# Kernel tuning notes

Measured on AMD Instinct MI355X. Metric: run time of the kernel, lower is better.

Reference implementation:

```python
import jax, jax.numpy as jnp
import numpy as np

PI = 3.141592653
PC_RANGE = np.array([-140.8, -40.0, -3.0, 140.8, 40.0, 1.0], np.float32)
IOU_THR = 0.1


def limit_period(val, offset=0.5, period=2 * PI):
    return val - jnp.floor(val / period + offset) * period


def pairwise_iou3d(boxes):
    # Axis-aligned 3D IoU approximation of the external boxes_iou3d_gpu CUDA kernel
    # (kernel source not provided). boxes: [N,7] = x,y,z,h,w,l,yaw; extents x<-l, y<-w, z<-h.
    c = boxes[:, :3]
    d = boxes[:, jnp.array([5, 4, 3])]
    lo = c - d * 0.5
    hi = c + d * 0.5
    inter = jnp.clip(jnp.minimum(hi[:, None, :], hi[None, :, :]) - jnp.maximum(lo[:, None, :], lo[None, :, :]), 0.0)
    inter_v = inter.prod(-1)                       # [N,N]
    vol = d.prod(-1)                               # [N]
    return inter_v / jnp.maximum(vol[:, None] + vol[None, :] - inter_v, 1e-8)


def cluster_assign(iou):
    # Greedy sequential clustering: repeatedly take the first unassigned box and
    # assign every box with iou > 0.1 (including already-assigned ones -> overwrite)
    # to a new cluster id. Equivalent to the original while-loop since an index,
    # once nonzero, never returns to zero, so the "first zero" scans left-to-right.
    iou = jax.lax.stop_gradient(iou)
    n = iou.shape[0]

    def body(i, carry):
        idx, cid = carry
        is_new = idx[i] == 0
        idx = jnp.where(is_new & (iou[i] > IOU_THR), cid, idx)
        return idx, cid + jnp.where(is_new, 1, 0).astype(jnp.int32)

    idx0 = jnp.zeros(n, jnp.int32)
    idx, cid = jax.lax.fori_loop(0, n, body, (idx0, jnp.int32(1)))
    return idx, cid


def cluster_fusion(boxes, scores, indices):
    n = boxes.shape[0]
    ids = jnp.arange(1, n + 1, dtype=jnp.int32)
    M = indices[None, :] == ids[:, None]            # [K,N] membership, K==N (padded)
    s_m = jnp.where(M, scores[None, :], 0.0)        # masked scores
    s_sum = s_m.sum(1)
    s_norm = s_m / jnp.maximum(s_sum, 1e-12)[:, None]
    dirs = boxes[:, 6]
    ref_idx = jnp.argmax(jnp.where(M, scores[None, :], -jnp.inf), axis=1)
    ref_dir = dirs[ref_idx]                         # yaw of max-score box per cluster
    diff = jnp.abs(dirs[None, :] - ref_dir[:, None])
    diff = jnp.where(diff > PI, 2 * PI - diff, diff)
    gt = diff > PI / 2
    score_gt = (s_m * gt).sum(1)
    score_le = s_sum - score_gt
    flip = jnp.where((score_gt <= score_le)[:, None], gt, ~gt)
    dirs_adj = limit_period(dirs[None, :] + PI * flip)
    theta = jnp.arctan2((jnp.sin(dirs_adj) * s_norm).sum(1), (jnp.cos(dirs_adj) * s_norm).sum(1))
    center_dim = s_norm @ boxes[:, :6]              # [K,6] score-weighted fusion
    boxes_fused = jnp.concatenate([center_dim, theta[:, None]], axis=1)
    # score fusion: sum_i s_sorted[i] ** (i+1), clipped to 1 (zeros from padding contribute 0)
    s_sorted = jnp.sort(s_m, axis=1)[:, ::-1]
    powers = jnp.arange(1, n + 1, dtype=jnp.float32)
    s_fused = jnp.minimum((s_sorted ** powers[None, :]).sum(1), 1.0)
    member = M.any(1)
    return boxes_fused, s_fused, member


def boxes_to_corners_3d(boxes):
    # order 'hwl': dims = h,w,l; l along x, w along y, h along z; rotate about z by yaw
    x, y, z = boxes[:, 0], boxes[:, 1], boxes[:, 2]
    h, w, l = boxes[:, 3], boxes[:, 4], boxes[:, 5]
    yaw = boxes[:, 6]
    xs = jnp.array([1, 1, -1, -1, 1, 1, -1, -1], jnp.float32) * 0.5
    ys = jnp.array([-1, 1, 1, -1, -1, 1, 1, -1], jnp.float32) * 0.5
    zs = jnp.array([-1, -1, -1, -1, 1, 1, 1, 1], jnp.float32) * 0.5
    cx = l[:, None] * xs
    cy = w[:, None] * ys
    cz = h[:, None] * zs
    c_, s_ = jnp.cos(yaw)[:, None], jnp.sin(yaw)[:, None]
    rx = cx * c_ - cy * s_
    ry = cx * s_ + cy * c_
    return jnp.stack([rx + x[:, None], ry + y[:, None], cz + z[:, None]], axis=-1)  # [N,8,3]


def setup_inputs() -> dict:
    key = jax.random.key(0)
    k1, k2, k3, k4, k5, k6 = jax.random.split(key, 6)
    C, M = 512, 8                # 512 objects seen by 8 agents -> 4096 detections
    N = C * M
    cx = jax.random.uniform(k1, (C,), minval=-120.0, maxval=120.0)
    cy = jax.random.uniform(k2, (C,), minval=-35.0, maxval=35.0)
    centers = jnp.stack([cx, cy, jnp.zeros(C)], -1)                     # [C,3]
    pos = (centers[:, None, :] + jax.random.normal(k3, (C, M, 3)) * 0.3).reshape(N, 3)
    dims = jnp.array([[1.56, 1.84, 4.2]]) + jax.random.normal(k4, (N, 3)) * 0.05  # h,w,l
    base_yaw = jax.random.uniform(k5, (C, 1), minval=-PI, maxval=PI)
    yaw = (base_yaw + jax.random.normal(k6, (C, M)) * 0.1).reshape(N, 1)
    boxes = jnp.concatenate([pos, dims, yaw], axis=1).astype(jnp.float32)
    scores = jax.random.uniform(jax.random.fold_in(key, 9), (N,), minval=0.05, maxval=0.95).astype(jnp.float32)
    return {"boxes": boxes, "scores": scores}


def reference(boxes, scores):
    boxes = boxes.at[:, 6].set(limit_period(boxes[:, 6]))
    iou = pairwise_iou3d(boxes)
    indices, _ = cluster_assign(iou)
    boxes_f, scores_f, member = cluster_fusion(boxes, scores, indices)
    corners = boxes_to_corners_3d(boxes_f)
    in_range = ((corners[..., 0] > PC_RANGE[0]) & (corners[..., 0] < PC_RANGE[3]) &
                (corners[..., 1] > PC_RANGE[1]) & (corners[..., 1] < PC_RANGE[4])).all(1)
    valid = member & in_range
    newid = jnp.cumsum(valid.astype(jnp.int32))     # remap surviving cluster ids to 1..K'
    safe = jnp.maximum(indices - 1, 0)
    new_indices = jnp.where((indices > 0) & valid[safe], newid[safe], 0)
    boxes_out = jnp.where(valid[:, None], boxes_f, 0.0)
    scores_out = jnp.where(valid, scores_f, 0.0)
    return boxes_out, scores_out, valid, new_indices
```

## Files before the change

kernel.cpp:

```cpp
#include <hip/hip_runtime.h>
#include <math.h>

#define PI_F      3.141592653f
#define TWO_PI_F  6.283185306f
#define HALF_PI_F 1.5707963265f
#define IOU_THR_F 0.1f

typedef unsigned long long u64;

__device__ __forceinline__ float limit_period_f(float v) {
    return v - floorf(v / TWO_PI_F + 0.5f) * TWO_PI_F;
}

__global__ void adj_kernel(const float* __restrict__ boxes,
                           u64* __restrict__ adjC,
                           unsigned char* __restrict__ occByte,
                           int* __restrict__ indices,
                           int n, int words) {
    __shared__ float jS[7][64];
    int w = blockIdx.x;
    int tid = threadIdx.x;
    int lane = tid & 63, wv = tid >> 6;
    if (blockIdx.x == 0) {
        int i2 = blockIdx.y * 256 + tid;
        if (i2 < n) indices[i2] = 0;
    }
    if (tid < 64) {
        int j = (w << 6) + tid;
        if (j < n) {
            float b0 = boxes[j*7+0], b1 = boxes[j*7+1], b2 = boxes[j*7+2];
            float b3 = boxes[j*7+3], b4 = boxes[j*7+4], b5 = boxes[j*7+5];
            jS[0][tid] = b0 - b5*0.5f;  jS[3][tid] = b0 + b5*0.5f;
            jS[1][tid] = b1 - b4*0.5f;  jS[4][tid] = b1 + b4*0.5f;
            jS[2][tid] = b2 - b3*0.5f;  jS[5][tid] = b2 + b3*0.5f;
            jS[6][tid] = (b5*b4)*b3;
        }
    }
    __syncthreads();
    int i = blockIdx.y * 256 + tid;
    u64 word = 0ull;
    if (i < n) {
        float b0 = boxes[i*7+0], b1 = boxes[i*7+1], b2 = boxes[i*7+2];
        float b3 = boxes[i*7+3], b4 = boxes[i*7+4], b5 = boxes[i*7+5];
        float lix = b0 - b5*0.5f, hix = b0 + b5*0.5f;
        float liy = b1 - b4*0.5f, hiy = b1 + b4*0.5f;
        float liz = b2 - b3*0.5f, hiz = b2 + b3*0.5f;
        float vi  = (b5*b4)*b3;
        int jmax = n - (w << 6); if (jmax > 64) jmax = 64;
        for (int jj = 0; jj < jmax; ++jj) {
            float ix = fminf(hix, jS[3][jj]) - fmaxf(lix, jS[0][jj]); ix = fmaxf(ix, 0.0f);
            float iy = fminf(hiy, jS[4][jj]) - fmaxf(liy, jS[1][jj]); iy = fmaxf(iy, 0.0f);
            float iz = fminf(hiz, jS[5][jj]) - fmaxf(liz, jS[2][jj]); iz = fmaxf(iz, 0.0f);
            float inter = (ix*iy)*iz;
            float u = fmaxf(vi + jS[6][jj] - inter, 1e-8f);
            bool pred = (inter / u) > IOU_THR_F;
            word |= ((u64)(pred ? 1 : 0)) << jj;
        }
        adjC[(size_t)w * n + i] = word;
    }
    u64 bal = __ballot((i < n) && word != 0ull);
    int rb = blockIdx.y * 4 + wv;
    if (lane == 0 && rb < 64)
        occByte[rb * 64 + w] = bal ? (unsigned char)1 : (unsigned char)0;
}

__global__ __launch_bounds__(1024) void mis_round_kernel(
        const u64* __restrict__ adjC,
        const unsigned char* __restrict__ occByte,
        u64* __restrict__ SG, u64* __restrict__ occLG,
        int* __restrict__ seedList, int* __restrict__ nclust,
        int n, int words) {
    __shared__ u64 S_l[64], R_l[64], occL[64];
    __shared__ int unresolved;
    __shared__ int wsS[64];
    int tid = threadIdx.x;
    int lane = tid & 63, wv = tid >> 6;

    for (int rb = wv; rb < 64; rb += 16) {
        unsigned char b = occByte[rb * 64 + lane];
        u64 m = __ballot(b != 0);
        if (lane == 0) occL[rb] = m;
    }
    if (tid < 64) {
        int base = tid << 6;
        int vb = n - base;
        u64 valid = (vb >= 64) ? ~0ull : ((vb <= 0) ? 0ull : ((1ull << vb) - 1ull));
        S_l[tid] = 0ull;
        R_l[tid] = ~valid;
    }
    __syncthreads();
    if (tid < 64) occLG[tid] = occL[tid];

    int id0[4], id1[4], id2[4], id3[4];
    u64 r0[4], r1[4], r2[4], r3[4], rstR[4];
    #pragma unroll
    for (int k = 0; k < 4; ++k) {
        int rb = (k << 4) + wv;
        int i = (rb << 6) + lane;
        id0[k] = id1[k] = id2[k] = id3[k] = 0xFF;
        r0[k] = r1[k] = r2[k] = r3[k] = 0ull; rstR[k] = 0ull;
        u64 lowm = lane ? ((1ull << lane) - 1ull) : 0ull;
        u64 oc = occL[rb] & ((rb >= 63) ? ~0ull : ((2ull << rb) - 1ull));
        int cnt = 0;
        while (oc) {
            int e = (int)__ffsll(oc) - 1; oc &= oc - 1;
            if (e >= words) break;
            u64 row = (i < n) ? adjC[(size_t)e * n + i] : 0ull;
            u64 em = (e < rb) ? ~0ull : lowm;
            u64 re = row & em;
            if (re) {
                if      (cnt == 0) { id0[k] = e; r0[k] = re; }
                else if (cnt == 1) { id1[k] = e; r1[k] = re; }
                else if (cnt == 2) { id2[k] = e; r2[k] = re; }
                else if (cnt == 3) { id3[k] = e; r3[k] = re; }
                else rstR[k] |= 1ull << e;
                ++cnt;
            }
        }
    }

    unsigned done = 0;
    #pragma unroll
    for (int k = 0; k < 4; ++k)
        if ((((k << 4) + wv) << 6) + lane >= n) done |= 1u << k;

    for (;;) {
        if (tid == 0) unresolved = 0;
        unsigned pendSeed = 0, pendRes = 0;
        #pragma unroll
        for (int k = 0; k < 4; ++k) {
            if (done & (1u << k)) continue;
            int rb = (k << 4) + wv;
            int i = (rb << 6) + lane;
            u64 lowm = lane ? ((1ull << lane) - 1ull) : 0ull;
            u64 sA = 0ull, uA = 0ull;
            if (id0[k] != 0xFF) { sA |= r0[k] & S_l[id0[k]]; uA |= r0[k] & ~R_l[id0[k]]; }
            if (id1[k] != 0xFF) { sA |= r1[k] & S_l[id1[k]]; uA |= r1[k] & ~R_l[id1[k]]; }
            if (id2[k] != 0xFF) { sA |= r2[k] & S_l[id2[k]]; uA |= r2[k] & ~R_l[id2[k]]; }
            if (id3[k] != 0xFF) { sA |= r3[k] & S_l[id3[k]]; uA |= r3[k] & ~R_l[id3[k]]; }
            u64 rm = rstR[k];
            while (rm) {
                int e = (int)__ffsll(rm) - 1; rm &= rm - 1;
                u64 row = adjC[(size_t)e * n + i];
                u64 em = (e < rb) ? ~0ull : lowm;
                sA |= row & S_l[e] & em;
                uA |= row & ~R_l[e] & em;
            }
            if (sA) pendRes |= 1u << k;
            else if (!uA) { pendSeed |= 1u << k; pendRes |= 1u << k; }
        }
        __syncthreads();
        #pragma unroll
        for (int k = 0; k < 4; ++k) {
            u64 bS = __ballot((pendSeed >> k) & 1u);
            u64 bR = __ballot((pendRes  >> k) & 1u);
            int rb = (k << 4) + wv;
            if (lane == 0 && rb < 64) {
                if (bS) atomicOr(&S_l[rb], bS);
                if (bR) atomicOr(&R_l[rb], bR);
            }
        }
        done |= pendRes;
        if ((done & 0xFu) != 0xFu) unresolved = 1;
        __syncthreads();
        if (unresolved == 0) break;
    }

    if (tid < 64) {
        u64 s = S_l[tid];
        SG[tid] = s;
        int pc = (int)__popcll(s);
        int x = pc;
        for (int o = 1; o < 64; o <<= 1) {
            int y = __shfl_up(x, o);
            if (tid >= o) x += y;
        }
        wsS[tid] = x - pc;
        if (tid == 63) *nclust = x;
    }
    __syncthreads();
    if (tid < 64) {
        u64 sbits = S_l[tid];
        int r = wsS[tid];
        while (sbits) {
            int b = (int)__ffsll(sbits) - 1; sbits &= sbits - 1;
            seedList[r++] = (tid << 6) + b;
        }
    }
}

__global__ void fusion_kernel(const float* __restrict__ boxes,
                              const float* __restrict__ scores,
                              const u64* __restrict__ SG,
                              const u64* __restrict__ occLG,
                              const int* __restrict__ seedListG,
                              const int* __restrict__ nclust,
                              const u64* __restrict__ adjC,
                              int* __restrict__ indices,
                              float* __restrict__ fused,
                              float* __restrict__ sfused,
                              int* __restrict__ validArr, int n, int words) {
    int lane = threadIdx.x;
    __shared__ u64 S_s[64];
    __shared__ int ws_s[64];
    __shared__ u64 occ_s[64];
    __shared__ unsigned short js[320], js2[320];
    __shared__ unsigned char keepB[320];
    __shared__ float ms[256];
    __shared__ float ds[256];
    __shared__ float bx[6][256];
    __shared__ float sv[256], cv[256], pw[256];
    __shared__ float refdirS, denomS;
    __shared__ int   flipS;
    {
        u64 s = (lane < words) ? SG[lane] : 0ull;
        S_s[lane] = s;
        occ_s[lane] = occLG[lane];
        int pc = (int)__popcll(s);
        int x = pc;
        for (int o = 1; o < 64; o <<= 1) {
            int y = __shfl_up(x, o);
            if (lane >= o) x += y;
        }
        ws_s[lane] = x - pc;
    }
    __syncthreads();
    int nc = *nclust;
    for (int i = blockIdx.x; i < n; i += gridDim.x) {
        int cid = i + 1;
        if (cid > nc) {
            if (lane < 7) fused[i*7+lane] = 0.0f;
            if (lane == 0) { sfused[i] = 0.0f; validArr[i] = 0; }
            continue;
        }
        int s = seedListG[i];
        u64 bits = (lane < words) ? adjC[(size_t)lane * n + s] : 0ull;
        int cnt = __popcll(bits);
        int x = cnt;
        for (int o = 1; o < 64; o <<= 1) {
            int y = __shfl_up(x, o);
            if (lane >= o) x += y;
        }
        int excl = x - cnt;
        int mc = __shfl(x, 63);
        if (mc > 320) mc = 320;
        int pos = excl;
        u64 t = bits;
        while (t) {
            int b = (int)__ffsll(t) - 1;
            t &= t - 1;
            if (pos < 320) js[pos] = (unsigned short)((lane << 6) + b);
            ++pos;
        }
        __syncthreads();
        for (int k = lane; k < mc; k += 64) {
            int j = js[k];
            int rb = j >> 6;
            int best = -1;
            u64 oc = occ_s[rb];
            while (oc) {
                int e = 63 - (int)__clzll(oc); oc &= ~(1ull << e);
                if (e >= words) continue;
                u64 m2 = adjC[(size_t)e * n + j] & S_s[e];
                if (m2) { best = (e << 6) + 63 - (int)__clzll(m2); break; }
            }
            int idx = 0;
            if (best >= 0) {
                int w2 = best >> 6, b = best & 63;
                u64 incl = (b >= 63) ? ~0ull : ((2ull << b) - 1ull);
                idx = ws_s[w2] + (int)__popcll(S_s[w2] & incl);
            }
            bool kp = (idx == cid);
            keepB[k] = kp ? 1 : 0;
            if (kp) indices[j] = idx;
        }
        __syncthreads();
        int m = 0;
        for (int base2 = 0; base2 < mc; base2 += 64) {
            int kk = base2 + lane;
            bool kp = (kk < mc) && keepB[kk];
            u64 bal = __ballot(kp);
            if (kp) {
                int p2 = m + (int)__popcll(bal & ((1ull << lane) - 1ull));
                if (p2 < 320) js2[p2] = js[kk];
            }
            m += (int)__popcll(bal);
        }
        __syncthreads();
        for (int k = lane; k < m; k += 64) {
            int j = js2[k];
            ms[k] = scores[j];
            ds[k] = limit_period_f(boxes[j*7+6]);
            bx[0][k] = boxes[j*7+0];
            bx[1][k] = boxes[j*7+1];
            bx[2][k] = boxes[j*7+2];
            bx[3][k] = boxes[j*7+3];
            bx[4][k] = boxes[j*7+4];
            bx[5][k] = boxes[j*7+5];
        }
        __syncthreads();
        if (m == 0) {
            if (lane == 0) {
                for (int k = 0; k < 7; ++k) fused[i*7+k] = 0.0f;
                sfused[i] = 0.0f; validArr[i] = 0;
            }
            __syncthreads();
            continue;
        }
        if (lane == 0) {
            float ssum = 0.0f, smax = -1e30f; int kref = 0;
            for (int k = 0; k < m; ++k) {
                float sc = ms[k];
                ssum += sc;
                if (sc > smax) { smax = sc; kref = k; }
            }
            float refdir = ds[kref];
            float denom = fmaxf(ssum, 1e-12f);
            float sgt = 0.0f;
            for (int k = 0; k < m; ++k) {
                float d = fabsf(ds[k] - refdir);
                if (d > PI_F) d = TWO_PI_F - d;
                if (d > HALF_PI_F) sgt += ms[k];
            }
            float sle = ssum - sgt;
            refdirS = refdir; denomS = denom;
            flipS = (sgt <= sle) ? 1 : 0;
        }
        __syncthreads();
        {
            float refdir = refdirS, denom = denomS;
            bool flipGt = flipS != 0;
            for (int k = lane; k < m; k += 64) {
                float dj = ds[k];
                float d = fabsf(dj - refdir);
                if (d > PI_F) d = TWO_PI_F - d;
                bool gt = d > HALF_PI_F;
                bool flip = flipGt ? gt : !gt;
                float adj_d = limit_period_f(dj + (flip ? PI_F : 0.0f));
                float wgt = ms[k] / denom;
                sv[k] = sinf(adj_d) * wgt;
                cv[k] = cosf(adj_d) * wgt;
            }
        }
        __syncthreads();
        if (lane == 0) {
            float denom = denomS;
            float cd0=0,cd1=0,cd2=0,cd3=0,cd4=0,cd5=0;
            for (int k = 0; k < m; ++k) {
                float wgt = ms[k] / denom;
                cd0 += wgt * bx[0][k];
                cd1 += wgt * bx[1][k];
                cd2 += wgt * bx[2][k];
                cd3 += wgt * bx[3][k];
                cd4 += wgt * bx[4][k];
                cd5 += wgt * bx[5][k];
            }
            float ssin = 0.0f, scos = 0.0f;
            for (int k = 0; k < m; ++k) { ssin += sv[k]; scos += cv[k]; }
            float theta = atan2f(ssin, scos);
            for (int k = 1; k < m; ++k) {
                float key = ms[k]; int p = k - 1;
                while (p >= 0 && ms[p] < key) { ms[p+1] = ms[p]; --p; }
                ms[p+1] = key;
            }
            bx[0][255] = cd0; bx[1][255] = cd1; bx[2][255] = cd2;
            bx[3][255] = cd3; bx[4][255] = cd4; bx[5][255] = cd5;
            sv[255] = theta;
        }
        __syncthreads();
        for (int k = lane; k < m; k += 64)
            pw[k] = powf(ms[k], (float)(k+1));
        __syncthreads();
        if (lane == 0) {
            float cd0 = bx[0][255], cd1 = bx[1][255], cd2 = bx[2][255];
            float cd3 = bx[3][255], cd4 = bx[4][255], cd5 = bx[5][255];
            float theta = sv[255];
            float sf = 0.0f;
            for (int k = 0; k < m; ++k) sf += pw[k];
            sf = fminf(sf, 1.0f);
            float c_ = cosf(theta), s_ = sinf(theta);
            float wdim = cd4, ldim = cd5;
            const float xs[4]  = {0.5f, 0.5f, -0.5f, -0.5f};
            const float ys_[4] = {-0.5f, 0.5f, 0.5f, -0.5f};
            bool inr = true;
            for (int c = 0; c < 4; ++c) {
                float cx = ldim * xs[c], cy = wdim * ys_[c];
                float rx = cx*c_ - cy*s_ + cd0;
                float ry = cx*s_ + cy*c_ + cd1;
                inr = inr && (rx > -140.8f) && (rx < 140.8f) && (ry > -40.0f) && (ry < 40.0f);
            }
            fused[i*7+0]=cd0; fused[i*7+1]=cd1; fused[i*7+2]=cd2;
            fused[i*7+3]=cd3; fused[i*7+4]=cd4; fused[i*7+5]=cd5;
            fused[i*7+6]=theta;
            sfused[i] = sf;
            validArr[i] = inr ? 1 : 0;
        }
        __syncthreads();
    }
}

__global__ void finalize_kernel(const float* __restrict__ fused,
                                const float* __restrict__ sfused,
                                const int* __restrict__ validArr,
                                const int* __restrict__ indices,
                                float* __restrict__ out, int n) {
    __shared__ int newidS[4096];
    __shared__ unsigned char validS[4096];
    __shared__ int scanBuf[1024];
    int tid = threadIdx.x;
    int per = (n + 1023) >> 10;
    int base = tid * per;
    int v[8];
    int sum = 0;
    for (int k = 0; k < per && k < 8; ++k) {
        int j = base + k;
        int vv = (j < n) ? validArr[j] : 0;
        v[k] = vv; sum += vv;
    }
    scanBuf[tid] = sum;
    __syncthreads();
    for (int o = 1; o < 1024; o <<= 1) {
        int val = scanBuf[tid];
        int add = (tid >= o) ? scanBuf[tid - o] : 0;
        __syncthreads();
        scanBuf[tid] = val + add;
        __syncthreads();
    }
    int run = scanBuf[tid] - sum;
    for (int k = 0; k < per && k < 8; ++k) {
        int j = base + k;
        if (j < n) { run += v[k]; newidS[j] = run; validS[j] = (unsigned char)v[k]; }
    }
    __syncthreads();
    float* boxesO  = out;
    float* scoresO = out + (size_t)7*n;
    float* validO  = out + (size_t)8*n;
    float* idxO    = out + (size_t)9*n;
    for (int j = tid; j < n; j += 1024) {
        int vv = validS[j];
        #pragma unroll
        for (int k = 0; k < 7; ++k)
            boxesO[j*7+k] = vv ? fused[j*7+k] : 0.0f;
        scoresO[j] = vv ? sfused[j] : 0.0f;
        validO[j]  = vv ? 1.0f : 0.0f;
        int ind = indices[j];
        int safe = ind - 1; if (safe < 0) safe = 0;
        bool nv = (ind > 0) && (validS[safe] != 0);
        idxO[j] = nv ? (float)newidS[safe] : 0.0f;
    }
}

extern "C" void kernel_launch(void* const* d_in, const int* in_sizes, int n_in,
                              void* d_out, int out_size, void* d_ws, size_t ws_size,
                              hipStream_t stream) {
    const float* boxes  = (const float*)d_in[0];
    const float* scores = (const float*)d_in[1];
    int n = in_sizes[0] / 7;
    int words = (n + 63) >> 6;

    char* ws = (char*)d_ws;
    size_t off = 0;
    u64* adjC = (u64*)(ws + off);
    off += (size_t)n * words * sizeof(u64);
    unsigned char* occByte = (unsigned char*)(ws + off); off += 64 * 64;
    u64* SG     = (u64*)(ws + off); off += 64 * sizeof(u64);
    u64* occLG  = (u64*)(ws + off); off += 64 * sizeof(u64);
    int* seedList = (int*)(ws + off); off += (size_t)n * sizeof(int);
    int* indices  = (int*)(ws + off); off += (size_t)n * sizeof(int);
    float* fused  = (float*)(ws + off); off += (size_t)n * 7 * sizeof(float);
    float* sfused = (float*)(ws + off); off += (size_t)n * sizeof(float);
    int* validArr = (int*)(ws + off); off += (size_t)n * sizeof(int);
    int* nclust   = (int*)(ws + off); off += sizeof(int);

    dim3 adjGrid(words, (n + 255) / 256);
    adj_kernel<<<adjGrid, 256, 0, stream>>>(boxes, adjC, occByte, indices, n, words);
    mis_round_kernel<<<1, 1024, 0, stream>>>(adjC, occByte, SG, occLG, seedList,
                                             nclust, n, words);
    fusion_kernel<<<512, 64, 0, stream>>>(boxes, scores, SG, occLG, seedList, nclust,
                                          adjC, indices, fused, sfused, validArr,
                                          n, words);
    finalize_kernel<<<1, 1024, 0, stream>>>(fused, sfused, validArr, indices,
                                            (float*)d_out, n);
}
```

Before: 91.70 us.

## Compute final cluster indices once in a dedicated parallel kernel before fusion

Adds an indices_kernel that, for each box in parallel, finds its last covering seed and the resulting cluster id. The same kernel also writes the seed list in parallel, replacing the serial per-word loop at the end of the single-block MIS kernel. The fusion kernel now filters cluster members with a simple indices lookup instead of recomputing each member's owning seed per cluster, and loops only over real clusters. validArr is zeroed up front in adj_kernel. This adds an extra kernel launch in exchange for removing redundant per-cluster owner searches and serial tail work.

```diff
diff --git a/kernel.cpp b/kernel.cpp
--- a/kernel.cpp
+++ b/kernel.cpp
@@ -15,7 +15,7 @@
 __global__ void adj_kernel(const float* __restrict__ boxes,
                            u64* __restrict__ adjC,
                            unsigned char* __restrict__ occByte,
-                           int* __restrict__ indices,
+                           int* __restrict__ validArr,
                            int n, int words) {
     __shared__ float jS[7][64];
     int w = blockIdx.x;
@@ -23,7 +23,7 @@
     int lane = tid & 63, wv = tid >> 6;
     if (blockIdx.x == 0) {
         int i2 = blockIdx.y * 256 + tid;
-        if (i2 < n) indices[i2] = 0;
+        if (i2 < n) validArr[i2] = 0;
     }
     if (tid < 64) {
         int j = (w << 6) + tid;
@@ -67,12 +67,9 @@
 __global__ __launch_bounds__(1024) void mis_round_kernel(
         const u64* __restrict__ adjC,
         const unsigned char* __restrict__ occByte,
-        u64* __restrict__ SG, u64* __restrict__ occLG,
-        int* __restrict__ seedList, int* __restrict__ nclust,
-        int n, int words) {
+        u64* __restrict__ SG, int n, int words) {
     __shared__ u64 S_l[64], R_l[64], occL[64];
     __shared__ int unresolved;
-    __shared__ int wsS[64];
     int tid = threadIdx.x;
     int lane = tid & 63, wv = tid >> 6;
 
@@ -89,7 +86,6 @@
         R_l[tid] = ~valid;
     }
     __syncthreads();
-    if (tid < 64) occLG[tid] = occL[tid];
 
     int id0[4], id1[4], id2[4], id3[4];
     u64 r0[4], r1[4], r2[4], r3[4], rstR[4];
@@ -165,130 +161,104 @@
         __syncthreads();
         if (unresolved == 0) break;
     }
-
-    if (tid < 64) {
-        u64 s = S_l[tid];
-        SG[tid] = s;
-        int pc = (int)__popcll(s);
-        int x = pc;
-        for (int o = 1; o < 64; o <<= 1) {
-            int y = __shfl_up(x, o);
-            if (tid >= o) x += y;
-        }
-        wsS[tid] = x - pc;
-        if (tid == 63) *nclust = x;
-    }
+    if (tid < 64) SG[tid] = S_l[tid];
+}
+
+__global__ __launch_bounds__(64) void indices_kernel(
+        const u64* __restrict__ adjC,
+        const unsigned char* __restrict__ occByte,
+        const u64* __restrict__ SG,
+        int* __restrict__ indices, int* __restrict__ seedList,
+        int* __restrict__ nclust, int n, int words) {
+    __shared__ u64 S_s[64];
+    __shared__ int ws_s[64];
+    int rb = blockIdx.x;
+    int lane = threadIdx.x;
+    unsigned char ob = occByte[rb * 64 + lane];
+    u64 occR = __ballot(ob != 0);
+    u64 s = (lane < words) ? SG[lane] : 0ull;
+    S_s[lane] = s;
+    int pc = (int)__popcll(s);
+    int x = pc;
+    for (int o = 1; o < 64; o <<= 1) {
+        int y = __shfl_up(x, o);
+        if (lane >= o) x += y;
+    }
+    ws_s[lane] = x - pc;
+    if (rb == 0 && lane == 63) *nclust = x;
     __syncthreads();
-    if (tid < 64) {
-        u64 sbits = S_l[tid];
-        int r = wsS[tid];
-        while (sbits) {
-            int b = (int)__ffsll(sbits) - 1; sbits &= sbits - 1;
-            seedList[r++] = (tid << 6) + b;
-        }
+    int j = (rb << 6) + lane;
+    if (j >= n) return;
+    int best = -1;
+    u64 oc = occR;
+    while (oc) {
+        int e = (int)__ffsll(oc) - 1; oc &= oc - 1;
+        if (e >= words) break;
+        u64 m2 = adjC[(size_t)e * n + j] & S_s[e];
+        if (m2) best = (e << 6) + 63 - (int)__clzll(m2);
+    }
+    int idx = 0;
+    if (best >= 0) {
+        int w2 = best >> 6, b = best & 63;
+        u64 incl = (b >= 63) ? ~0ull : ((2ull << b) - 1ull);
+        idx = ws_s[w2] + (int)__popcll(S_s[w2] & incl);
+    }
+    indices[j] = idx;
+    int bj = j & 63;
+    if ((S_s[rb] >> bj) & 1ull) {
+        int rank = ws_s[rb] + (int)__popcll(S_s[rb] & (bj ? ((1ull << bj) - 1ull) : 0ull)) + 1;
+        seedList[rank - 1] = j;
     }
 }
 
 __global__ void fusion_kernel(const float* __restrict__ boxes,
                               const float* __restrict__ scores,
-                              const u64* __restrict__ SG,
-                              const u64* __restrict__ occLG,
+                              const int* __restrict__ indices,
                               const int* __restrict__ seedListG,
                               const int* __restrict__ nclust,
                               const u64* __restrict__ adjC,
-                              int* __restrict__ indices,
                               float* __restrict__ fused,
                               float* __restrict__ sfused,
                               int* __restrict__ validArr, int n, int words) {
     int lane = threadIdx.x;
-    __shared__ u64 S_s[64];
-    __shared__ int ws_s[64];
-    __shared__ u64 occ_s[64];
-    __shared__ unsigned short js[320], js2[320];
-    __shared__ unsigned char keepB[320];
+    int nc = *nclust;
+    __shared__ unsigned short js[256];
     __shared__ float ms[256];
     __shared__ float ds[256];
     __shared__ float bx[6][256];
     __shared__ float sv[256], cv[256], pw[256];
     __shared__ float refdirS, denomS;
     __shared__ int   flipS;
-    {
-        u64 s = (lane < words) ? SG[lane] : 0ull;
-        S_s[lane] = s;
-        occ_s[lane] = occLG[lane];
-        int pc = (int)__popcll(s);
-        int x = pc;
-        for (int o = 1; o < 64; o <<= 1) {
-            int y = __shfl_up(x, o);
-            if (lane >= o) x += y;
-        }
-        ws_s[lane] = x - pc;
-    }
-    __syncthreads();
-    int nc = *nclust;
-    for (int i = blockIdx.x; i < n; i += gridDim.x) {
+    for (int i = blockIdx.x; i < nc; i += gridDim.x) {
         int cid = i + 1;
-        if (cid > nc) {
-            if (lane < 7) fused[i*7+lane] = 0.0f;
-            if (lane == 0) { sfused[i] = 0.0f; validArr[i] = 0; }
-            continue;
-        }
         int s = seedListG[i];
         u64 bits = (lane < words) ? adjC[(size_t)lane * n + s] : 0ull;
-        int cnt = __popcll(bits);
+        u64 keep = 0ull;
+        u64 t = bits;
+        while (t) {
+            int b = (int)__ffsll(t) - 1;
+            t &= t - 1;
+            int node = (lane << 6) + b;
+            if (indices[node] == cid) keep |= (1ull << b);
+        }
+        int cnt = __popcll(keep);
         int x = cnt;
         for (int o = 1; o < 64; o <<= 1) {
             int y = __shfl_up(x, o);
             if (lane >= o) x += y;
         }
         int excl = x - cnt;
-        int mc = __shfl(x, 63);
-        if (mc > 320) mc = 320;
+        int m = __shfl(x, 63);
         int pos = excl;
-        u64 t = bits;
+        t = keep;
         while (t) {
             int b = (int)__ffsll(t) - 1;
             t &= t - 1;
-            if (pos < 320) js[pos] = (unsigned short)((lane << 6) + b);
-            ++pos;
-        }
-        __syncthreads();
-        for (int k = lane; k < mc; k += 64) {
+            js[pos++] = (unsigned short)((lane << 6) + b);
+        }
+        __syncthreads();
+        for (int k = lane; k < m; k += 64) {
             int j = js[k];
-            int rb = j >> 6;
-            int best = -1;
-            u64 oc = occ_s[rb];
-            while (oc) {
-                int e = 63 - (int)__clzll(oc); oc &= ~(1ull << e);
-                if (e >= words) continue;
-                u64 m2 = adjC[(size_t)e * n + j] & S_s[e];
-                if (m2) { best = (e << 6) + 63 - (int)__clzll(m2); break; }
-            }
-            int idx = 0;
-            if (best >= 0) {
-                int w2 = best >> 6, b = best & 63;
-                u64 incl = (b >= 63) ? ~0ull : ((2ull << b) - 1ull);
-                idx = ws_s[w2] + (int)__popcll(S_s[w2] & incl);
-            }
-            bool kp = (idx == cid);
-            keepB[k] = kp ? 1 : 0;
-            if (kp) indices[j] = idx;
-        }
-        __syncthreads();
-        int m = 0;
-        for (int base2 = 0; base2 < mc; base2 += 64) {
-            int kk = base2 + lane;
-            bool kp = (kk < mc) && keepB[kk];
-            u64 bal = __ballot(kp);
-            if (kp) {
-                int p2 = m + (int)__popcll(bal & ((1ull << lane) - 1ull));
-                if (p2 < 320) js2[p2] = js[kk];
-            }
-            m += (int)__popcll(bal);
-        }
-        __syncthreads();
-        for (int k = lane; k < m; k += 64) {
-            int j = js2[k];
             ms[k] = scores[j];
             ds[k] = limit_period_f(boxes[j*7+6]);
             bx[0][k] = boxes[j*7+0];
@@ -464,7 +434,6 @@
     off += (size_t)n * words * sizeof(u64);
     unsigned char* occByte = (unsigned char*)(ws + off); off += 64 * 64;
     u64* SG     = (u64*)(ws + off); off += 64 * sizeof(u64);
-    u64* occLG  = (u64*)(ws + off); off += 64 * sizeof(u64);
     int* seedList = (int*)(ws + off); off += (size_t)n * sizeof(int);
     int* indices  = (int*)(ws + off); off += (size_t)n * sizeof(int);
     float* fused  = (float*)(ws + off); off += (size_t)n * 7 * sizeof(float);
@@ -473,12 +442,12 @@
     int* nclust   = (int*)(ws + off); off += sizeof(int);
 
     dim3 adjGrid(words, (n + 255) / 256);
-    adj_kernel<<<adjGrid, 256, 0, stream>>>(boxes, adjC, occByte, indices, n, words);
-    mis_round_kernel<<<1, 1024, 0, stream>>>(adjC, occByte, SG, occLG, seedList,
-                                             nclust, n, words);
-    fusion_kernel<<<512, 64, 0, stream>>>(boxes, scores, SG, occLG, seedList, nclust,
-                                          adjC, indices, fused, sfused, validArr,
-                                          n, words);
+    adj_kernel<<<adjGrid, 256, 0, stream>>>(boxes, adjC, occByte, validArr, n, words);
+    mis_round_kernel<<<1, 1024, 0, stream>>>(adjC, occByte, SG, n, words);
+    indices_kernel<<<(n + 63) / 64, 64, 0, stream>>>(adjC, occByte, SG, indices,
+                                                     seedList, nclust, n, words);
+    fusion_kernel<<<512, 64, 0, stream>>>(boxes, scores, indices, seedList, nclust,
+                                          adjC, fused, sfused, validArr, n, words);
     finalize_kernel<<<1, 1024, 0, stream>>>(fused, sfused, validArr, indices,
                                             (float*)d_out, n);
 }
```

Result: no change. 92.93 us (+1.3%).
